# Performance work log

Measured on AMD Instinct MI355X. Metric: run time of the kernel, lower is better.

The kernel has to match this reference:

```python
import jax, jax.numpy as jnp
import numpy as np

D_MODEL = 1024
N_HEADS = 16
D_FF = 4096
LN_EPS = 1e-5


def _linear_params(key, d_in, d_out):
    kw, kb = jax.random.split(key)
    bound = 1.0 / np.sqrt(d_in)
    W = jax.random.uniform(kw, (d_out, d_in), jnp.float32, -bound, bound)
    b = jax.random.uniform(kb, (d_out,), jnp.float32, -bound, bound)
    return W, b


def setup_inputs() -> dict:
    key = jax.random.key(0)
    ks = jax.random.split(key, 8)
    x = jax.random.normal(ks[0], (2, 2048, D_MODEL), jnp.float32)
    Wq, bq = _linear_params(ks[1], D_MODEL, D_MODEL)
    Wk, bk = _linear_params(ks[2], D_MODEL, D_MODEL)
    Wv, bv = _linear_params(ks[3], D_MODEL, D_MODEL)
    Wo, bo = _linear_params(ks[4], D_MODEL, D_MODEL)
    W1, b1 = _linear_params(ks[5], D_MODEL, D_FF)
    W2, b2 = _linear_params(ks[6], D_FF, D_MODEL)
    ln1_g = jnp.ones((D_MODEL,), jnp.float32)
    ln1_b = jnp.zeros((D_MODEL,), jnp.float32)
    ln2_g = jnp.ones((D_MODEL,), jnp.float32)
    ln2_b = jnp.zeros((D_MODEL,), jnp.float32)
    return dict(x=x, Wq=Wq, bq=bq, Wk=Wk, bk=bk, Wv=Wv, bv=bv, Wo=Wo, bo=bo,
                ln1_g=ln1_g, ln1_b=ln1_b, W1=W1, b1=b1, W2=W2, b2=b2,
                ln2_g=ln2_g, ln2_b=ln2_b)


def _layernorm(x, g, b):
    mu = jnp.mean(x, axis=-1, keepdims=True)
    var = jnp.mean(jnp.square(x - mu), axis=-1, keepdims=True)
    return (x - mu) * jax.lax.rsqrt(var + LN_EPS) * g + b


def _lin(x, W, b):
    return jnp.einsum('bsd,ed->bse', x, W) + b


def _attn(x, Wq, bq, Wk, bk, Wv, bv, Wo, bo):
    B, S, _ = x.shape
    d_head = D_MODEL // N_HEADS
    scale = d_head ** -0.5
    split = lambda t: t.reshape(B, S, N_HEADS, d_head).transpose(0, 2, 1, 3)
    q = split(_lin(x, Wq, bq))  # b h s d
    k = split(_lin(x, Wk, bk))
    v = split(_lin(x, Wv, bv))
    scores = jnp.einsum('bhqd,bhkd->bhqk', q, k) * scale
    attn = jax.nn.softmax(scores, axis=-1)
    out = jnp.einsum('bhqk,bhkd->bhqd', attn, v)
    out = out.transpose(0, 2, 1, 3).reshape(B, S, D_MODEL)
    return _lin(out, Wo, bo)


def reference(x, Wq, bq, Wk, bk, Wv, bv, Wo, bo, ln1_g, ln1_b, W1, b1, W2, b2, ln2_g, ln2_b):
    x = x + _attn(_layernorm(x, ln1_g, ln1_b), Wq, bq, Wk, bk, Wv, bv, Wo, bo)
    h = _layernorm(x, ln2_g, ln2_b)
    h = _lin(h, W1, b1)
    h = jax.nn.gelu(h, approximate=False)
    h = _lin(h, W2, b2)
    return x + h
```

## Files before the change

kernel.cpp:

```cpp
#include <hip/hip_runtime.h>
#include <hip/hip_bf16.h>
#include <stdint.h>

#define DM 1024
#define DFF 4096
#define NH 16
#define DH 64
#define SEQ 2048
#define MROWS 4096

typedef unsigned short u16;
typedef __attribute__((ext_vector_type(8))) short bf16x8;
typedef __attribute__((ext_vector_type(4))) float f32x4;
typedef __attribute__((ext_vector_type(16))) float f32x16;
typedef __attribute__((ext_vector_type(4))) unsigned short u16x4;

__device__ __forceinline__ u16 f2b(float f) {
  union { float f; uint32_t u; } v; v.f = f;
  uint32_t r = v.u + 0x7FFFu + ((v.u >> 16) & 1u);
  return (u16)(r >> 16);
}

__device__ __forceinline__ u16 f2bn(float f) {
  __hip_bfloat16 h = __float2bfloat16(f);
  return *reinterpret_cast<u16*>(&h);
}

__device__ __forceinline__ uint32_t pk2(float lo, float hi) {
  return (uint32_t)f2bn(lo) | ((uint32_t)f2bn(hi) << 16);
}

__device__ __forceinline__ void gl_lds16(const void* g, void* l) {
  __builtin_amdgcn_global_load_lds(
      (const __attribute__((address_space(1))) uint32_t*)g,
      (__attribute__((address_space(3))) uint32_t*)l, 16, 0, 0);
}

struct CvtArgs { const float* src[6]; u16* dst[6]; int n4[6]; };

__global__ void cvt_kernel(CvtArgs a) {
  const int stride = gridDim.x * blockDim.x;
  const int t0 = blockIdx.x * blockDim.x + threadIdx.x;
  for (int i = 0; i < 6; ++i) {
    const float4* s = (const float4*)a.src[i];
    u16x4* d = (u16x4*)a.dst[i];
    const int n = a.n4[i];
    for (int idx = t0; idx < n; idx += stride) {
      float4 v = s[idx];
      u16x4 o;
      o[0] = f2b(v.x); o[1] = f2b(v.y); o[2] = f2b(v.z); o[3] = f2b(v.w);
      d[idx] = o;
    }
  }
}

__global__ __launch_bounds__(256)
void ln_kernel(const float* __restrict__ x, const float* __restrict__ g,
               const float* __restrict__ be, u16* __restrict__ out) {
  const int row = blockIdx.x;
  const int tid = threadIdx.x;
  const float4 v = ((const float4*)(x + (size_t)row * DM))[tid];
  float s  = v.x + v.y + v.z + v.w;
  float s2 = v.x * v.x + v.y * v.y + v.z * v.z + v.w * v.w;
  #pragma unroll
  for (int m = 1; m < 64; m <<= 1) {
    s  += __shfl_xor(s,  m, 64);
    s2 += __shfl_xor(s2, m, 64);
  }
  __shared__ float red[8];
  const int w = tid >> 6, lane = tid & 63;
  if (lane == 0) { red[w] = s; red[4 + w] = s2; }
  __syncthreads();
  s  = red[0] + red[1] + red[2] + red[3];
  s2 = red[4] + red[5] + red[6] + red[7];
  const float mu  = s * (1.0f / DM);
  const float var = s2 * (1.0f / DM) - mu * mu;
  const float rstd = rsqrtf(var + 1e-5f);
  const float4 gv = ((const float4*)g)[tid];
  const float4 bv = ((const float4*)be)[tid];
  u16x4 o;
  o[0] = f2b((v.x - mu) * rstd * gv.x + bv.x);
  o[1] = f2b((v.y - mu) * rstd * gv.y + bv.y);
  o[2] = f2b((v.z - mu) * rstd * gv.z + bv.z);
  o[3] = f2b((v.w - mu) * rstd * gv.w + bv.w);
  ((u16x4*)(out + (size_t)row * DM))[tid] = o;
}

__global__ __launch_bounds__(256)
void combine_kernel(const float4* __restrict__ p0, const float4* __restrict__ p1,
                    const float4* __restrict__ bias, const float4* __restrict__ resid,
                    float4* __restrict__ out, int total4, int colmask4) {
  for (int i = blockIdx.x * 256 + threadIdx.x; i < total4; i += gridDim.x * 256) {
    float4 a = p0[i], b = p1[i], bs = bias[i & colmask4], rr = resid[i];
    float4 o;
    o.x = a.x + b.x + bs.x + rr.x;
    o.y = a.y + b.y + bs.y + rr.y;
    o.z = a.z + b.z + bs.z + rr.z;
    o.w = a.w + b.w + bs.w + rr.w;
    out[i] = o;
  }
}

__global__ __launch_bounds__(256)
void combine_ln_kernel(const float4* __restrict__ p0, const float4* __restrict__ p1,
                       const float4* __restrict__ bias, const float4* __restrict__ resid,
                       float4* __restrict__ xout,
                       const float* __restrict__ g, const float* __restrict__ be,
                       u16* __restrict__ nout) {
  const int row = blockIdx.x;
  const int tid = threadIdx.x;
  const int i = row * (DM / 4) + tid;
  const float4 a = p0[i], b = p1[i], bs = bias[tid], rr = resid[i];
  float4 v;
  v.x = a.x + b.x + bs.x + rr.x;
  v.y = a.y + b.y + bs.y + rr.y;
  v.z = a.z + b.z + bs.z + rr.z;
  v.w = a.w + b.w + bs.w + rr.w;
  xout[i] = v;
  float s  = v.x + v.y + v.z + v.w;
  float s2 = v.x * v.x + v.y * v.y + v.z * v.z + v.w * v.w;
  #pragma unroll
  for (int m = 1; m < 64; m <<= 1) {
    s  += __shfl_xor(s,  m, 64);
    s2 += __shfl_xor(s2, m, 64);
  }
  __shared__ float red[8];
  const int w = tid >> 6, lane = tid & 63;
  if (lane == 0) { red[w] = s; red[4 + w] = s2; }
  __syncthreads();
  s  = red[0] + red[1] + red[2] + red[3];
  s2 = red[4] + red[5] + red[6] + red[7];
  const float mu  = s * (1.0f / DM);
  const float var = s2 * (1.0f / DM) - mu * mu;
  const float rstd = rsqrtf(var + 1e-5f);
  const float4 gv = ((const float4*)g)[tid];
  const float4 bv = ((const float4*)be)[tid];
  u16x4 o;
  o[0] = f2b((v.x - mu) * rstd * gv.x + bv.x);
  o[1] = f2b((v.y - mu) * rstd * gv.y + bv.y);
  o[2] = f2b((v.z - mu) * rstd * gv.z + bv.z);
  o[3] = f2b((v.w - mu) * rstd * gv.w + bv.w);
  ((u16x4*)(nout + (size_t)row * DM))[tid] = o;
}

struct GemmPtrs { const u16* W[3]; const float* bias[3]; void* out[3];
                  const float* resid; int vtrans; };

template<int EPI>
__global__ __launch_bounds__(256)
void gemm_bt(const u16* __restrict__ A, GemmPtrs p, int M, int N,
             int Kstride, int Kchunk) {
  __shared__ __align__(16) u16 As[128 * 64];
  __shared__ __align__(16) u16 Bs[128 * 64];
  const u16* __restrict__ Wm = p.W[blockIdx.z];
  const float* __restrict__ bias = p.bias[blockIdx.z];
  void* outv = p.out[blockIdx.z];
  const float* resid = p.resid;

  const int tid = threadIdx.x;
  const int lane = tid & 63;
  const int w = tid >> 6;
  const int brow = blockIdx.y * 128;
  const int bcol = blockIdx.x * 128;
  const int wr = (w >> 1) * 64, wc = (w & 1) * 64;
  const int koff = (EPI == 3) ? blockIdx.z * Kchunk : 0;

  f32x4 acc[4][4] = {};

  const int srow = lane >> 3;
  const int scol = (lane & 7) * 8;
  const int nkt = Kchunk >> 6;
  for (int kt = 0; kt < nkt; ++kt) {
    const int k0 = koff + kt * 64;
    #pragma unroll
    for (int i = 0; i < 4; ++i) {
      const int r = i * 32 + w * 8;
      gl_lds16(&A [(size_t)(brow + r + srow) * Kstride + k0 + scol], &As[r * 64]);
      gl_lds16(&Wm[(size_t)(bcol + r + srow) * Kstride + k0 + scol], &Bs[r * 64]);
    }
    __syncthreads();
    #pragma unroll
    for (int ks = 0; ks < 2; ++ks) {
      const int ko = ks * 32 + (lane >> 4) * 8;
      bf16x8 a[4], b[4];
      #pragma unroll
      for (int f = 0; f < 4; ++f)
        a[f] = *(const bf16x8*)&As[(wr + f * 16 + (lane & 15)) * 64 + ko];
      #pragma unroll
      for (int f = 0; f < 4; ++f)
        b[f] = *(const bf16x8*)&Bs[(wc + f * 16 + (lane & 15)) * 64 + ko];
      #pragma unroll
      for (int fr = 0; fr < 4; ++fr)
        #pragma unroll
        for (int fc = 0; fc < 4; ++fc)
          acc[fr][fc] = __builtin_amdgcn_mfma_f32_16x16x32_bf16(a[fr], b[fc], acc[fr][fc], 0, 0, 0);
    }
    __syncthreads();
  }

  const int orow0 = brow + wr + (lane >> 4) * 4;
  const int ocol0 = bcol + wc + (lane & 15);

  if (EPI == 0 && p.vtrans && blockIdx.z == 2) {
    #pragma unroll
    for (int fr = 0; fr < 4; ++fr) {
      const int row0 = orow0 + fr * 16;
      const int bq = row0 >> 11, s0 = row0 & (SEQ - 1);
      #pragma unroll
      for (int fc = 0; fc < 4; ++fc) {
        const int col = ocol0 + fc * 16;
        const float bvv = bias[col];
        u16x4 o;
        #pragma unroll
        for (int r = 0; r < 4; ++r) o[r] = f2b(acc[fr][fc][r] + bvv);
        *(u16x4*)((u16*)outv + (size_t)(bq * DM + col) * SEQ + s0) = o;
      }
    }
    return;
  }

  const float oscale = (EPI == 0 && p.vtrans && blockIdx.z == 0) ? 0.125f : 1.0f;

  #pragma unroll
  for (int fr = 0; fr < 4; ++fr) {
    #pragma unroll
    for (int fc = 0; fc < 4; ++fc) {
      const int col = ocol0 + fc * 16;
      const float bvv = (EPI == 3) ? 0.0f : bias[col];
      #pragma unroll
      for (int r = 0; r < 4; ++r) {
        const int row = orow0 + fr * 16 + r;
        const size_t idx = (size_t)row * N + col;
        float v = acc[fr][fc][r] + bvv;
        if (EPI == 0) {
          ((u16*)outv)[idx] = f2b(v * oscale);
        } else if (EPI == 1) {
          float ge = 0.5f * v * (1.0f + erff(v * 0.70710678118654752f));
          ((u16*)outv)[idx] = f2b(ge);
        } else if (EPI == 2) {
          ((float*)outv)[idx] = v + resid[idx];
        } else {
          ((float*)outv)[idx] = v;
        }
      }
    }
  }
}

__global__ __launch_bounds__(128, 4)
void attn_kernel(const u16* __restrict__ Q, const u16* __restrict__ K,
                 const u16* __restrict__ Vt, u16* __restrict__ O) {
  __shared__ __align__(16) u16 Ks[64 * 64];
  __shared__ __align__(16) u16 Vts[64 * 64];
  const int tid = threadIdx.x, lane = tid & 63, w = tid >> 6;
  const int bh = blockIdx.y, b = bh >> 4, h = bh & 15;
  const int q0 = blockIdx.x * 64 + w * 32;
  const size_t base = (size_t)b * SEQ * DM + (size_t)h * DH;
  const size_t vbase = (size_t)(b * DM + h * DH) * SEQ;

  const int l31 = lane & 31, hi = lane >> 5, l7 = l31 & 7;

  bf16x8 qf[4];
  {
    const size_t qrow = base + (size_t)(q0 + l31) * DM;
    #pragma unroll
    for (int dt = 0; dt < 4; ++dt)
      qf[dt] = *(const bf16x8*)&Q[qrow + dt * 16 + hi * 8];
  }

  f32x16 oacc[2] = {};
  float mq = -1e30f, lq = 0.0f;

  for (int kt = 0; kt < SEQ / 64; ++kt) {
    #pragma unroll
    for (int i = 0; i < 4; ++i) {
      const int r0 = w * 32 + i * 8;
      const int row = r0 + (lane >> 3);
      const int ch = ((lane & 7) ^ (row & 7)) * 8;
      gl_lds16(&K[base + (size_t)(kt * 64 + row) * DM + ch], &Ks[r0 * 64]);
      gl_lds16(&Vt[vbase + (size_t)row * SEQ + kt * 64 + ch], &Vts[r0 * 64]);
    }
    __syncthreads();

    #pragma unroll
    for (int sub = 0; sub < 2; ++sub) {
      f32x16 sacc = {};
      __builtin_amdgcn_s_setprio(1);
      #pragma unroll
      for (int dt = 0; dt < 4; ++dt) {
        bf16x8 kf = *(const bf16x8*)&Ks[(sub * 32 + l31) * 64 + (((dt << 1) | hi) ^ l7) * 8];
        sacc = __builtin_amdgcn_mfma_f32_32x32x16_bf16(kf, qf[dt], sacc, 0, 0, 0);
      }
      __builtin_amdgcn_s_setprio(0);

      float tm = sacc[0];
      #pragma unroll
      for (int r = 1; r < 16; ++r) tm = fmaxf(tm, sacc[r]);
      tm = fmaxf(tm, __shfl_xor(tm, 32, 64));

      if (__any(tm > mq + 8.0f)) {
        const float mnew = fmaxf(mq, tm);
        const float fs = __expf(mq - mnew);
        mq = mnew;
        lq *= fs;
        #pragma unroll
        for (int r = 0; r < 16; ++r) {
          const float fsr = __shfl(fs, (r & 3) + 8 * (r >> 2) + 4 * hi, 64);
          oacc[0][r] *= fsr;
          oacc[1][r] *= fsr;
        }
      }

      uint32_t wd[2][4];
      float ps = 0.0f;
      #pragma unroll
      for (int half = 0; half < 2; ++half) {
        float p[8];
        #pragma unroll
        for (int j = 0; j < 8; ++j) {
          p[j] = __expf(sacc[half * 8 + j] - mq);
          ps += p[j];
        }
        const uint32_t a = pk2(p[0], p[1]), c = pk2(p[2], p[3]);
        const uint32_t bb = pk2(p[4], p[5]), d = pk2(p[6], p[7]);
        const uint32_t xa = (uint32_t)__shfl_xor((int)a, 32, 64);
        const uint32_t xb = (uint32_t)__shfl_xor((int)bb, 32, 64);
        const uint32_t xc = (uint32_t)__shfl_xor((int)c, 32, 64);
        const uint32_t xd = (uint32_t)__shfl_xor((int)d, 32, 64);
        wd[half][0] = hi ? xb : a;
        wd[half][1] = hi ? xd : c;
        wd[half][2] = hi ? bb : xa;
        wd[half][3] = hi ? d : xc;
      }
      lq += ps;
      bf16x8 pa0, pa1;
      #pragma unroll
      for (int j = 0; j < 4; ++j) {
        ((uint32_t*)&pa0)[j] = wd[0][j];
        ((uint32_t*)&pa1)[j] = wd[1][j];
      }

      __builtin_amdgcn_s_setprio(1);
      #pragma unroll
      for (int dt = 0; dt < 2; ++dt) {
        #pragma unroll
        for (int ks = 0; ks < 2; ++ks) {
          bf16x8 vf = *(const bf16x8*)&Vts[(dt * 32 + l31) * 64 +
                                           (((sub << 2) | (ks << 1) | hi) ^ l7) * 8];
          oacc[dt] = __builtin_amdgcn_mfma_f32_32x32x16_bf16(ks ? pa1 : pa0, vf, oacc[dt], 0, 0, 0);
        }
      }
      __builtin_amdgcn_s_setprio(0);
    }
    __syncthreads();
  }

  const float ltot = lq + __shfl_xor(lq, 32, 64);
  #pragma unroll
  for (int r = 0; r < 16; ++r) {
    const int crow = (r & 3) + 8 * (r >> 2) + 4 * hi;
    const float lr = __shfl(ltot, crow, 64);
    const float inv = 1.0f / lr;
    const size_t orow = base + (size_t)(q0 + crow) * DM;
    O[orow + l31]      = f2bn(oacc[0][r] * inv);
    O[orow + 32 + l31] = f2bn(oacc[1][r] * inv);
  }
}

extern "C" void kernel_launch(void* const* d_in, const int* in_sizes, int n_in,
                              void* d_out, int out_size, void* d_ws, size_t ws_size,
                              hipStream_t stream) {
  const float* x    = (const float*)d_in[0];
  const float* Wq   = (const float*)d_in[1];
  const float* bq   = (const float*)d_in[2];
  const float* Wk   = (const float*)d_in[3];
  const float* bk   = (const float*)d_in[4];
  const float* Wv   = (const float*)d_in[5];
  const float* bv   = (const float*)d_in[6];
  const float* Wo   = (const float*)d_in[7];
  const float* bo   = (const float*)d_in[8];
  const float* ln1g = (const float*)d_in[9];
  const float* ln1b = (const float*)d_in[10];
  const float* W1   = (const float*)d_in[11];
  const float* b1   = (const float*)d_in[12];
  const float* W2   = (const float*)d_in[13];
  const float* b2   = (const float*)d_in[14];
  const float* ln2g = (const float*)d_in[15];
  const float* ln2b = (const float*)d_in[16];
  float* out = (float*)d_out;

  char* wsb = (char*)d_ws;
  size_t off = 0;
  auto alloc = [&](size_t bytes) -> char* {
    char* pp = wsb + off;
    off += (bytes + 255) & ~(size_t)255;
    return pp;
  };
  u16* Wq_b = (u16*)alloc((size_t)DM * DM * 2);
  u16* Wk_b = (u16*)alloc((size_t)DM * DM * 2);
  u16* Wv_b = (u16*)alloc((size_t)DM * DM * 2);
  u16* Wo_b = (u16*)alloc((size_t)DM * DM * 2);
  u16* W1_b = (u16*)alloc((size_t)DFF * DM * 2);
  u16* W2_b = (u16*)alloc((size_t)DM * DFF * 2);
  u16* xn   = (u16*)alloc((size_t)MROWS * DM * 2);
  u16* qb   = (u16*)alloc((size_t)MROWS * DM * 2);
  u16* kb   = (u16*)alloc((size_t)MROWS * DM * 2);
  u16* vt   = (u16*)alloc((size_t)MROWS * DM * 2);
  u16* ao   = (u16*)alloc((size_t)MROWS * DM * 2);
  u16* h1   = (u16*)alloc((size_t)MROWS * DFF * 2);

  float* pA = (float*)xn;
  float* pB = (float*)kb;

  CvtArgs ca;
  ca.src[0] = Wq; ca.dst[0] = Wq_b; ca.n4[0] = DM * DM / 4;
  ca.src[1] = Wk; ca.dst[1] = Wk_b; ca.n4[1] = DM * DM / 4;
  ca.src[2] = Wv; ca.dst[2] = Wv_b; ca.n4[2] = DM * DM / 4;
  ca.src[3] = Wo; ca.dst[3] = Wo_b; ca.n4[3] = DM * DM / 4;
  ca.src[4] = W1; ca.dst[4] = W1_b; ca.n4[4] = DFF * DM / 4;
  ca.src[5] = W2; ca.dst[5] = W2_b; ca.n4[5] = DM * DFF / 4;
  cvt_kernel<<<2048, 256, 0, stream>>>(ca);

  ln_kernel<<<MROWS, 256, 0, stream>>>(x, ln1g, ln1b, xn);

  GemmPtrs pq = {};
  pq.W[0] = Wq_b; pq.W[1] = Wk_b; pq.W[2] = Wv_b;
  pq.bias[0] = bq; pq.bias[1] = bk; pq.bias[2] = bv;
  pq.out[0] = qb; pq.out[1] = kb; pq.out[2] = vt;
  pq.vtrans = 1;
  gemm_bt<0><<<dim3(DM / 128, MROWS / 128, 3), 256, 0, stream>>>(xn, pq, MROWS, DM, DM, DM);

  attn_kernel<<<dim3(SEQ / 64, 2 * NH), 128, 0, stream>>>(qb, kb, vt, ao);

  GemmPtrs po = {};
  po.W[0] = Wo_b; po.W[1] = Wo_b;
  po.bias[0] = bo; po.bias[1] = bo;
  po.out[0] = pA; po.out[1] = pB;
  gemm_bt<3><<<dim3(DM / 128, MROWS / 128, 2), 256, 0, stream>>>(ao, po, MROWS, DM, DM, DM / 2);
  combine_ln_kernel<<<MROWS, 256, 0, stream>>>((const float4*)pA, (const float4*)pB,
                                               (const float4*)bo, (const float4*)x,
                                               (float4*)out, ln2g, ln2b, ao);

  GemmPtrs p1 = {};
  p1.W[0] = W1_b; p1.bias[0] = b1; p1.out[0] = h1;
  gemm_bt<1><<<dim3(DFF / 128, MROWS / 128, 1), 256, 0, stream>>>(ao, p1, MROWS, DFF, DM, DM);

  GemmPtrs p2 = {};
  p2.W[0] = W2_b; p2.W[1] = W2_b;
  p2.bias[0] = b2; p2.bias[1] = b2;
  p2.out[0] = pA; p2.out[1] = pB;
  gemm_bt<3><<<dim3(DM / 128, MROWS / 128, 2), 256, 0, stream>>>(h1, p2, MROWS, DM, DFF, DFF / 2);
  combine_kernel<<<2048, 256, 0, stream>>>((const float4*)pA, (const float4*)pB,
                                           (const float4*)b2, (const float4*)out,
                                           (float4*)out, MROWS * DM / 4, DM / 4 - 1);
}
```

Before: 317.1 us.

## Split attention over KV halves and merge partial results in a separate kernel

The attention kernel gains a third grid dimension that splits the key/value sequence into two halves. Each block writes unnormalized fp32 partial outputs plus its running max and sum, and a new merge kernel rescales and combines the two halves into the bf16 output. The aim is more parallelism, since the grid was 32x32 blocks of 128 threads. The cost is extra fp32 partial traffic (reusing the h1 buffer), an additional launch, and a second pass over the data.

```diff
diff --git a/kernel.cpp b/kernel.cpp
--- a/kernel.cpp
+++ b/kernel.cpp
@@ -249,14 +249,18 @@
 
 __global__ __launch_bounds__(128, 4)
 void attn_kernel(const u16* __restrict__ Q, const u16* __restrict__ K,
-                 const u16* __restrict__ Vt, u16* __restrict__ O) {
+                 const u16* __restrict__ Vt, float* __restrict__ Opart,
+                 float2* __restrict__ ML) {
   __shared__ __align__(16) u16 Ks[64 * 64];
   __shared__ __align__(16) u16 Vts[64 * 64];
   const int tid = threadIdx.x, lane = tid & 63, w = tid >> 6;
   const int bh = blockIdx.y, b = bh >> 4, h = bh & 15;
+  const int kvh = blockIdx.z;
   const int q0 = blockIdx.x * 64 + w * 32;
   const size_t base = (size_t)b * SEQ * DM + (size_t)h * DH;
   const size_t vbase = (size_t)(b * DM + h * DH) * SEQ;
+  float* __restrict__ Op = Opart + (size_t)kvh * MROWS * DM;
+  float2* __restrict__ mlp = ML + (size_t)kvh * 2 * NH * SEQ;
 
   const int l31 = lane & 31, hi = lane >> 5, l7 = l31 & 7;
 
@@ -271,7 +275,7 @@
   f32x16 oacc[2] = {};
   float mq = -1e30f, lq = 0.0f;
 
-  for (int kt = 0; kt < SEQ / 64; ++kt) {
+  for (int kt = kvh * (SEQ / 128); kt < (kvh + 1) * (SEQ / 128); ++kt) {
     #pragma unroll
     for (int i = 0; i < 4; ++i) {
       const int r0 = w * 32 + i * 8;
@@ -359,12 +363,32 @@
   #pragma unroll
   for (int r = 0; r < 16; ++r) {
     const int crow = (r & 3) + 8 * (r >> 2) + 4 * hi;
-    const float lr = __shfl(ltot, crow, 64);
-    const float inv = 1.0f / lr;
     const size_t orow = base + (size_t)(q0 + crow) * DM;
-    O[orow + l31]      = f2bn(oacc[0][r] * inv);
-    O[orow + 32 + l31] = f2bn(oacc[1][r] * inv);
-  }
+    Op[orow + l31]      = oacc[0][r];
+    Op[orow + 32 + l31] = oacc[1][r];
+  }
+  if (hi == 0) mlp[(size_t)bh * SEQ + q0 + l31] = make_float2(mq, ltot);
+}
+
+__global__ __launch_bounds__(256)
+void attn_merge(const float4* __restrict__ Op0, const float4* __restrict__ Op1,
+                const float2* __restrict__ ML, u16* __restrict__ ao) {
+  const int row = blockIdx.x, tid = threadIdx.x;
+  const int idx4 = row * (DM / 4) + tid;
+  const int bh = ((row >> 11) << 4) | (tid >> 4);
+  const int s = row & (SEQ - 1);
+  const float2 a = ML[(size_t)bh * SEQ + s];
+  const float2 c = ML[(size_t)(2 * NH) * SEQ + (size_t)bh * SEQ + s];
+  const float m = fmaxf(a.x, c.x);
+  const float f0 = __expf(a.x - m), f1 = __expf(c.x - m);
+  const float inv = 1.0f / (a.y * f0 + c.y * f1);
+  const float4 o0 = Op0[idx4], o1 = Op1[idx4];
+  u16x4 o;
+  o[0] = f2bn((o0.x * f0 + o1.x * f1) * inv);
+  o[1] = f2bn((o0.y * f0 + o1.y * f1) * inv);
+  o[2] = f2bn((o0.z * f0 + o1.z * f1) * inv);
+  o[3] = f2bn((o0.w * f0 + o1.w * f1) * inv);
+  ((u16x4*)ao)[idx4] = o;
 }
 
 extern "C" void kernel_launch(void* const* d_in, const int* in_sizes, int n_in,
@@ -408,9 +432,11 @@
   u16* vt   = (u16*)alloc((size_t)MROWS * DM * 2);
   u16* ao   = (u16*)alloc((size_t)MROWS * DM * 2);
   u16* h1   = (u16*)alloc((size_t)MROWS * DFF * 2);
+  float2* ml = (float2*)alloc((size_t)2 * 2 * NH * SEQ * sizeof(float2));
 
   float* pA = (float*)xn;
   float* pB = (float*)kb;
+  float* attnOp = (float*)h1;
 
   CvtArgs ca;
   ca.src[0] = Wq; ca.dst[0] = Wq_b; ca.n4[0] = DM * DM / 4;
@@ -430,7 +456,10 @@
   pq.vtrans = 1;
   gemm_bt<0><<<dim3(DM / 128, MROWS / 128, 3), 256, 0, stream>>>(xn, pq, MROWS, DM, DM, DM);
 
-  attn_kernel<<<dim3(SEQ / 64, 2 * NH), 128, 0, stream>>>(qb, kb, vt, ao);
+  attn_kernel<<<dim3(SEQ / 64, 2 * NH, 2), 128, 0, stream>>>(qb, kb, vt, attnOp, ml);
+  attn_merge<<<MROWS, 256, 0, stream>>>((const float4*)attnOp,
+                                        (const float4*)(attnOp + (size_t)MROWS * DM),
+                                        (const float2*)ml, ao);
 
   GemmPtrs po = {};
   po.W[0] = Wo_b; po.W[1] = Wo_b;
```

Measured after the change: 304.5 us. 3.9% less time.
